# Optimization experiments

Hardware: AMD Instinct MI355X
Metric: run time of the kernel (lower is better)

Reference implementation:

```python
import jax, jax.numpy as jnp
import numpy as np

B, S, D = 128, 50, 128
NUM_NODE = 40000
SAMPLE = 12
HOP = 2
ALPHA = 0.2  # leaky-relu slope (opt.alpha)


def _leaky(x, slope=ALPHA):
    return jnp.where(x >= 0, x, slope * x)


def setup_inputs() -> dict:
    key = jax.random.key(0)
    ks = jax.random.split(key, 12)
    stdv = 1.0 / float(np.sqrt(D))
    inputs = jax.random.randint(ks[0], (B, S), 0, NUM_NODE)
    adj = jax.random.randint(ks[1], (B, S, S), 0, 5)
    mask_item = jax.random.randint(ks[2], (B, S), 0, 2).at[:, 0].set(1)
    item = jax.random.randint(ks[3], (B, S), 0, NUM_NODE)
    adj_all = jax.random.randint(ks[4], (NUM_NODE, SAMPLE), 0, NUM_NODE)
    num_weight = jax.random.uniform(ks[5], (NUM_NODE, SAMPLE), dtype=jnp.float32)
    embedding = jax.random.uniform(ks[6], (NUM_NODE, D), minval=-stdv, maxval=stdv, dtype=jnp.float32)
    a_local = jax.random.uniform(ks[7], (4, D), minval=-stdv, maxval=stdv, dtype=jnp.float32)
    agg_w1 = jax.random.uniform(ks[8], (HOP, D + 1, D), minval=-stdv, maxval=stdv, dtype=jnp.float32)
    agg_w2 = jax.random.uniform(ks[9], (HOP, D, 1), minval=-stdv, maxval=stdv, dtype=jnp.float32)
    agg_w3 = jax.random.uniform(ks[10], (HOP, 2 * D, D), minval=-stdv, maxval=stdv, dtype=jnp.float32)
    return dict(inputs=inputs, adj=adj, mask_item=mask_item, item=item,
                adj_all=adj_all, num_weight=num_weight, embedding=embedding,
                a_local=a_local, agg_w1=agg_w1, agg_w2=agg_w2, agg_w3=agg_w3)


def _local_agg(h, adj, a_local):
    # e_k[b,i,j] = leakyrelu(sum_d h[b,i,d]*h[b,j,d]*a_k[d]); never materialize [B,N,N,D]
    e = _leaky(jnp.einsum('bid,bjd,kd->kbij', h, h, a_local))  # [4,B,S,S]
    alpha = jnp.full(e.shape[1:], -9e15, dtype=h.dtype)
    for k in range(4):
        alpha = jnp.where(adj == k + 1, e[k], alpha)
    alpha = jax.nn.softmax(alpha, axis=-1)
    return alpha @ h


def _global_agg(w1, w2, w3, self_v, neigh_v, neigh_w, extra):
    # self_v [B,L,D]; neigh_v [B,L,SAMPLE,D]; neigh_w [B,L,SAMPLE]; extra [B,L,D]
    feat = jnp.concatenate([extra[:, :, None, :] * neigh_v, neigh_w[..., None]], axis=-1)  # [B,L,SAMPLE,D+1]
    a = _leaky(feat @ w1, 0.2)                              # [B,L,SAMPLE,D]
    a = jax.nn.softmax((a @ w2)[..., 0], axis=-1)[..., None]  # [B,L,SAMPLE,1]
    neigh = jnp.sum(a * neigh_v, axis=-2)                   # [B,L,D]
    out = jnp.concatenate([self_v, neigh], axis=-1) @ w3    # [B,L,D]
    return jax.nn.relu(out)


def _forward(inputs, adj, mask_item, item, adj_all, num_weight, embedding,
             a_local, agg_w1, agg_w2, agg_w3):
    h = embedding[inputs]                          # [B,S,D]
    h_local = _local_agg(h, adj, a_local)
    # multi-hop neighbor sampling (index_select into adj_all / num)
    item_neighbors = [inputs]
    weight_neighbors = []
    support = S
    for _ in range(HOP):
        last = item_neighbors[-1].reshape(-1)
        support *= SAMPLE
        item_neighbors.append(adj_all[last].reshape(B, support))
        weight_neighbors.append(num_weight[last].reshape(B, support))
    entity = [embedding[idx] for idx in item_neighbors]
    mask_f = mask_item.astype(h.dtype)
    item_emb = embedding[item] * mask_f[..., None]
    session = (jnp.sum(item_emb, 1) / jnp.sum(mask_f, -1, keepdims=True))[:, None, :]  # [B,1,D]
    for n_hop in range(HOP):
        nxt = []
        for hop in range(HOP - n_hop):
            self_v = entity[hop]
            L = self_v.shape[1]
            neigh_v = entity[hop + 1].reshape(B, L, SAMPLE, D)
            neigh_w = weight_neighbors[hop].reshape(B, L, SAMPLE)
            extra = jnp.broadcast_to(session, (B, L, D))
            nxt.append(_global_agg(agg_w1[n_hop], agg_w2[n_hop], agg_w3[n_hop],
                                   self_v, neigh_v, neigh_w, extra))
        entity = nxt
    h_global = entity[0].reshape(B, S, D)
    # dropout_local / dropout_global are identity in eval mode
    return h_local + h_global


def reference(inputs, adj, mask_item, item, adj_all, num_weight, embedding,
              a_local, agg_w1, agg_w2, agg_w3):
    return _forward(inputs, adj, mask_item, item, adj_all, num_weight, embedding,
                    a_local, agg_w1, agg_w2, agg_w3)
```

## Files before the change

### kernel.cpp

```cpp
#include <hip/hip_runtime.h>
#include <math.h>

#define BATCH 128
#define S 50
#define D 128
#define SAMPLE 12
#define NL 8

typedef __attribute__((ext_vector_type(8))) short short8v;
typedef __attribute__((ext_vector_type(4))) float f32x4;

__device__ __forceinline__ float leakyf(float x) { return x >= 0.f ? x : 0.2f * x; }
__device__ __forceinline__ unsigned short f2bf(float f) {
    union { float f; unsigned int u; } v; v.f = f;
    unsigned int u = v.u;
    return (unsigned short)((u + 0x7FFFu + ((u >> 16) & 1u)) >> 16);
}
__device__ __forceinline__ float bf2f(unsigned short h) {
    union { float f; unsigned int u; } v; v.u = ((unsigned int)h) << 16; return v.f;
}

__global__ __launch_bounds__(256) void local_agg_kernel(
    const int* __restrict__ inputs, const int* __restrict__ adj,
    const float* __restrict__ emb, const float* __restrict__ a_local,
    float* __restrict__ out)
{
    __shared__ float h[S][D];
    __shared__ float al[4][D];
    __shared__ float alpha[S][S];
    const int b = blockIdx.x;
    const int t = threadIdx.x;

    for (int idx = t; idx < S * D; idx += 256) {
        int i = idx / D, d = idx % D;
        h[i][d] = emb[inputs[b * S + i] * D + d];
    }
    for (int idx = t; idx < 4 * D; idx += 256) al[idx / D][idx % D] = a_local[idx];
    __syncthreads();

    for (int p = t; p < S * S; p += 256) {
        int i = p / S, j = p % S;
        int a = adj[b * S * S + p];
        float v = -9e15f;
        if (a >= 1 && a <= 4) {
            const float* ak = al[a - 1];
            float dot = 0.f;
            #pragma unroll 4
            for (int d = 0; d < D; ++d) dot += h[i][d] * h[j][d] * ak[d];
            v = leakyf(dot);
        }
        alpha[i][j] = v;
    }
    __syncthreads();

    if (t < S) {
        float m = -INFINITY;
        for (int j = 0; j < S; ++j) m = fmaxf(m, alpha[t][j]);
        float ssum = 0.f;
        for (int j = 0; j < S; ++j) { float e = expf(alpha[t][j] - m); alpha[t][j] = e; ssum += e; }
        float inv = 1.f / ssum;
        for (int j = 0; j < S; ++j) alpha[t][j] *= inv;
    }
    __syncthreads();

    for (int idx = t; idx < S * D; idx += 256) {
        int i = idx / D, d = idx % D;
        float acc = 0.f;
        #pragma unroll 5
        for (int j = 0; j < S; ++j) acc += alpha[i][j] * h[j][d];
        out[b * S * D + idx] = acc;
    }
}

__global__ __launch_bounds__(128) void session_kernel(
    const int* __restrict__ item, const int* __restrict__ mask,
    const float* __restrict__ emb, float* __restrict__ session)
{
    const int b = blockIdx.x, d = threadIdx.x;
    float num = 0.f, den = 0.f;
    for (int s = 0; s < S; ++s) {
        float m = (float)mask[b * S + s];
        num += m * emb[item[b * S + s] * D + d];
        den += m;
    }
    session[b * D + d] = num / den;
}

__global__ __launch_bounds__(256) void n1_kernel(
    const int* __restrict__ inputs, const int* __restrict__ adj_all,
    int* __restrict__ n1)
{
    int idx = blockIdx.x * 256 + threadIdx.x;
    if (idx >= BATCH * 600) return;
    int b = idx / 600, j = idx % 600;
    int node = inputs[b * S + j / SAMPLE];
    n1[idx] = adj_all[node * SAMPLE + j % SAMPLE];
}

__global__ __launch_bounds__(256) void prep_kernel(
    const float* __restrict__ w1, const float* __restrict__ w3,
    unsigned short* __restrict__ w1t, unsigned short* __restrict__ w3t)
{
    int idx = blockIdx.x * 256 + threadIdx.x;
    if (idx < 2 * 128 * 128) {
        int h = idx >> 14, r = idx & 16383, n = r >> 7, k = r & 127;
        w1t[idx] = f2bf(w1[h * 129 * 128 + k * 128 + n]);
    } else {
        int j = idx - 2 * 128 * 128;
        int h = j >> 15, r = j & 32767, n = r >> 8, k = r & 255;
        w3t[j] = f2bf(w3[h * 256 * 128 + k * 128 + n]);
    }
}

template <int MODE>
__global__ __launch_bounds__(256, 2) void global_kernel(
    const int* __restrict__ inputs, const int* __restrict__ adj_all,
    const float* __restrict__ num_weight, const float* __restrict__ emb,
    const int* __restrict__ n1, const float* __restrict__ session,
    const unsigned short* __restrict__ ent_self, const unsigned short* __restrict__ ent_neigh,
    const unsigned short* __restrict__ w1t, const float* __restrict__ w1,
    const float* __restrict__ w2, const unsigned short* __restrict__ w3t,
    unsigned short* __restrict__ outb, float* __restrict__ outf, int L)
{
    __shared__ unsigned short nvL[96 * 128];
    __shared__ unsigned short A2[16 * 256];
    __shared__ float score_w[4][96];
    __shared__ float score[96];
    __shared__ float sessL[128];
    __shared__ float w1lastL[128];
    __shared__ float nwgtL[96];
    __shared__ int   selfNode[8];
    __shared__ int   neighIdx[96];

    const int b = blockIdx.y;
    const int l0 = blockIdx.x * NL;
    const int t = threadIdx.x;
    const int lane = t & 63;
    const int wv = t >> 6;
    const int cn = lane & 15;
    const int cg = lane >> 4;

    if (t < 128) sessL[t] = session[b * 128 + t];
    else         w1lastL[t - 128] = w1[128 * 128 + (t - 128)];
    if (t < 8) {
        int l = l0 + t;
        selfNode[t] = (l < L) ? ((MODE == 1) ? n1[b * 600 + l] : inputs[b * S + l]) : -1;
    }
    __syncthreads();

    if (t < 96) {
        int li = t / SAMPLE, s2 = t % SAMPLE;
        int node = selfNode[li];
        int row = -1; float wgt = 0.f;
        if (node >= 0) {
            if (MODE == 0)      row = n1[b * 600 + (l0 + li) * SAMPLE + s2];
            else if (MODE == 1) row = adj_all[node * SAMPLE + s2];
            else                row = b * 600 + (l0 + li) * SAMPLE + s2;
            wgt = num_weight[node * SAMPLE + s2];
        }
        neighIdx[t] = row; nwgtL[t] = wgt;
    }
    reinterpret_cast<float4*>((char*)A2 + 8 * 512)[t] = make_float4(0.f, 0.f, 0.f, 0.f);
    __syncthreads();

    for (int q = t; q < 96 * 32; q += 256) {
        int m = q >> 5, dq = q & 31;
        int row = neighIdx[m];
        ushort4 bv = make_ushort4(0, 0, 0, 0);
        if (row >= 0) {
            if (MODE == 2) {
                bv = reinterpret_cast<const ushort4*>(ent_neigh)[row * 32 + dq];
            } else {
                float4 v = reinterpret_cast<const float4*>(emb)[row * 32 + dq];
                bv.x = f2bf(v.x); bv.y = f2bf(v.y); bv.z = f2bf(v.z); bv.w = f2bf(v.w);
            }
        }
        unsigned byteoff = m * 256 + ((dq * 8) ^ ((m & 7) << 4));
        *reinterpret_cast<ushort4*>((char*)nvL + byteoff) = bv;
    }
    {
        int li = t >> 5, dq = t & 31;
        int l = l0 + li;
        ushort4 bv = make_ushort4(0, 0, 0, 0);
        if (l < L) {
            if (MODE == 2) {
                bv = reinterpret_cast<const ushort4*>(ent_self)[(b * 50 + l) * 32 + dq];
            } else {
                float4 v = reinterpret_cast<const float4*>(emb)[selfNode[li] * 32 + dq];
                bv.x = f2bf(v.x); bv.y = f2bf(v.y); bv.z = f2bf(v.z); bv.w = f2bf(v.w);
            }
        }
        unsigned byteoff = li * 512 + ((dq * 8) ^ ((li & 7) << 4));
        *reinterpret_cast<ushort4*>((char*)A2 + byteoff) = bv;
    }
    __syncthreads();

    f32x4 acc[6][2];
    #pragma unroll
    for (int mt = 0; mt < 6; ++mt)
        #pragma unroll
        for (int j = 0; j < 2; ++j)
            acc[mt][j] = (f32x4){0.f, 0.f, 0.f, 0.f};

    #pragma unroll
    for (int kk = 0; kk < 4; ++kk) {
        int kbase = kk * 32 + cg * 8;
        short8v bfr[2];
        #pragma unroll
        for (int j = 0; j < 2; ++j) {
            int n = (2 * wv + j) * 16 + cn;
            short8v braw = *reinterpret_cast<const short8v*>(w1t + n * 128 + kbase);
            short8v bs;
            #pragma unroll
            for (int e = 0; e < 8; ++e) {
                float f = bf2f((unsigned short)braw[e]) * sessL[kbase + e];
                bs[e] = (short)f2bf(f);
            }
            bfr[j] = bs;
        }
        #pragma unroll
        for (int mt = 0; mt < 6; ++mt) {
            unsigned byteoff = (mt * 16 + cn) * 256 + ((kbase * 2) ^ ((cn & 7) << 4));
            short8v a = *reinterpret_cast<const short8v*>((const char*)nvL + byteoff);
            acc[mt][0] = __builtin_amdgcn_mfma_f32_16x16x32_bf16(a, bfr[0], acc[mt][0], 0, 0, 0);
            acc[mt][1] = __builtin_amdgcn_mfma_f32_16x16x32_bf16(a, bfr[1], acc[mt][1], 0, 0, 0);
        }
    }

    {
        float w2v0 = w2[(2 * wv) * 16 + cn];
        float w2v1 = w2[(2 * wv + 1) * 16 + cn];
        float w1l0 = w1lastL[(2 * wv) * 16 + cn];
        float w1l1 = w1lastL[(2 * wv + 1) * 16 + cn];
        #pragma unroll
        for (int mt = 0; mt < 6; ++mt) {
            #pragma unroll
            for (int r = 0; r < 4; ++r) {
                float nw = nwgtL[mt * 16 + cg * 4 + r];
                float z0 = acc[mt][0][r] + nw * w1l0;
                float z1 = acc[mt][1][r] + nw * w1l1;
                float v = leakyf(z0) * w2v0 + leakyf(z1) * w2v1;
                v += __shfl_xor(v, 1); v += __shfl_xor(v, 2);
                v += __shfl_xor(v, 4); v += __shfl_xor(v, 8);
                if (cn == 0) score_w[wv][mt * 16 + cg * 4 + r] = v;
            }
        }
    }
    __syncthreads();

    if (t < 8) {
        float e[SAMPLE]; float mx = -INFINITY;
        #pragma unroll
        for (int s2 = 0; s2 < SAMPLE; ++s2) {
            int m = t * SAMPLE + s2;
            float v = score_w[0][m] + score_w[1][m] + score_w[2][m] + score_w[3][m];
            e[s2] = v; mx = fmaxf(mx, v);
        }
        float ssum = 0.f;
        #pragma unroll
        for (int s2 = 0; s2 < SAMPLE; ++s2) { e[s2] = expf(e[s2] - mx); ssum += e[s2]; }
        float inv = 1.f / ssum;
        #pragma unroll
        for (int s2 = 0; s2 < SAMPLE; ++s2) score[t * SAMPLE + s2] = e[s2] * inv;
    }
    __syncthreads();

    #pragma unroll
    for (int i = 0; i < 4; ++i) {
        int idx = i * 256 + t;
        int l = idx >> 7, d = idx & 127;
        float a = 0.f;
        #pragma unroll
        for (int s2 = 0; s2 < SAMPLE; ++s2) {
            int m = l * SAMPLE + s2;
            unsigned byteoff = m * 256 + ((2 * d) ^ ((m & 7) << 4));
            a += score[m] * bf2f(*reinterpret_cast<const unsigned short*>((const char*)nvL + byteoff));
        }
        unsigned ob = l * 512 + ((2 * (128 + d)) ^ ((l & 7) << 4));
        *reinterpret_cast<unsigned short*>((char*)A2 + ob) = f2bf(a);
    }
    __syncthreads();

    f32x4 acc2[2];
    acc2[0] = (f32x4){0.f, 0.f, 0.f, 0.f};
    acc2[1] = (f32x4){0.f, 0.f, 0.f, 0.f};
    #pragma unroll
    for (int kk = 0; kk < 8; ++kk) {
        int kbase = kk * 32 + cg * 8;
        unsigned ab = cn * 512 + ((kbase * 2) ^ ((cn & 7) << 4));
        short8v a = *reinterpret_cast<const short8v*>((const char*)A2 + ab);
        #pragma unroll
        for (int j = 0; j < 2; ++j) {
            int n = (2 * wv + j) * 16 + cn;
            short8v bb = *reinterpret_cast<const short8v*>(w3t + n * 256 + kbase);
            acc2[j] = __builtin_amdgcn_mfma_f32_16x16x32_bf16(a, bb, acc2[j], 0, 0, 0);
        }
    }
    #pragma unroll
    for (int j = 0; j < 2; ++j) {
        int n = (2 * wv + j) * 16 + cn;
        #pragma unroll
        for (int r = 0; r < 4; ++r) {
            int rowi = cg * 4 + r;
            if (rowi < 8 && (l0 + rowi) < L) {
                float val = fmaxf(acc2[j][r], 0.f);
                if (MODE == 2) {
                    float* p = outf + ((size_t)(b * 50) + l0 + rowi) * 128 + n;
                    *p = val + *p;
                } else {
                    outb[((size_t)b * L + l0 + rowi) * 128 + n] = f2bf(val);
                }
            }
        }
    }
}

extern "C" void kernel_launch(void* const* d_in, const int* in_sizes, int n_in,
                              void* d_out, int out_size, void* d_ws, size_t ws_size,
                              hipStream_t stream)
{
    const int*   inputs     = (const int*)d_in[0];
    const int*   adj        = (const int*)d_in[1];
    const int*   mask_item  = (const int*)d_in[2];
    const int*   item       = (const int*)d_in[3];
    const int*   adj_all    = (const int*)d_in[4];
    const float* num_weight = (const float*)d_in[5];
    const float* embedding  = (const float*)d_in[6];
    const float* a_local    = (const float*)d_in[7];
    const float* agg_w1     = (const float*)d_in[8];
    const float* agg_w2     = (const float*)d_in[9];
    const float* agg_w3     = (const float*)d_in[10];
    float* out = (float*)d_out;

    float*          ws_session = (float*)d_ws;
    int*            ws_n1      = (int*)(ws_session + 16384);
    unsigned short* ws_w1t     = (unsigned short*)(ws_n1 + 76800);
    unsigned short* ws_w3t     = ws_w1t + 2 * 128 * 128;
    unsigned short* ws_out0    = ws_w3t + 2 * 128 * 256;
    unsigned short* ws_out1    = ws_out0 + (size_t)BATCH * 50 * D;

    prep_kernel<<<dim3(384), 256, 0, stream>>>(agg_w1, agg_w3, ws_w1t, ws_w3t);
    local_agg_kernel<<<dim3(BATCH), 256, 0, stream>>>(inputs, adj, embedding, a_local, out);
    session_kernel<<<dim3(BATCH), 128, 0, stream>>>(item, mask_item, embedding, ws_session);
    n1_kernel<<<dim3(300), 256, 0, stream>>>(inputs, adj_all, ws_n1);

    global_kernel<0><<<dim3(7, BATCH), 256, 0, stream>>>(
        inputs, adj_all, num_weight, embedding, ws_n1, ws_session,
        nullptr, nullptr, ws_w1t, agg_w1, agg_w2, ws_w3t, ws_out0, nullptr, 50);
    global_kernel<1><<<dim3(75, BATCH), 256, 0, stream>>>(
        inputs, adj_all, num_weight, embedding, ws_n1, ws_session,
        nullptr, nullptr, ws_w1t, agg_w1, agg_w2, ws_w3t, ws_out1, nullptr, 600);
    global_kernel<2><<<dim3(7, BATCH), 256, 0, stream>>>(
        inputs, adj_all, num_weight, embedding, ws_n1, ws_session,
        ws_out0, ws_out1, ws_w1t + 128 * 128, agg_w1 + 129 * 128,
        agg_w2 + 128, ws_w3t + 128 * 256, nullptr, out, 50);
}
```

Measured before the change: 355.5 us.

## Fuse local and hop-0 global kernels, pre-convert embedding and session-scaled W1 to bf16

Replaces the seven launches with four. Session and n1 are merged into one setup kernel. A prep kernel converts the whole embedding table to bf16 and builds per-batch session-scaled W1 tiles. The local aggregation and both hop-0 global paths share one launch, picked by block index. Gathers become 16-byte bf16 loads, the B fragments no longer need per-element rescaling, the weighted-sum loop handles two values per thread, and occupancy is raised to 4 blocks per CU. In exchange, the whole 40000x128 table is converted every call, which costs about 30MB of traffic.

```diff
diff --git a/kernel.cpp b/kernel.cpp
--- a/kernel.cpp
+++ b/kernel.cpp
@@ -5,146 +5,171 @@
 #define S 50
 #define D 128
 #define SAMPLE 12
-#define NL 8
 
 typedef __attribute__((ext_vector_type(8))) short short8v;
 typedef __attribute__((ext_vector_type(4))) float f32x4;
+typedef unsigned short u16;
 
 __device__ __forceinline__ float leakyf(float x) { return x >= 0.f ? x : 0.2f * x; }
-__device__ __forceinline__ unsigned short f2bf(float f) {
-    union { float f; unsigned int u; } v; v.f = f;
-    unsigned int u = v.u;
-    return (unsigned short)((u + 0x7FFFu + ((u >> 16) & 1u)) >> 16);
-}
-__device__ __forceinline__ float bf2f(unsigned short h) {
-    union { float f; unsigned int u; } v; v.u = ((unsigned int)h) << 16; return v.f;
-}
-
-__global__ __launch_bounds__(256) void local_agg_kernel(
+__device__ __forceinline__ u16 f2bf(float f) {
+    union { float f; unsigned u; } v; v.f = f;
+    unsigned u = v.u;
+    return (u16)((u + 0x7FFFu + ((u >> 16) & 1u)) >> 16);
+}
+__device__ __forceinline__ float bf2f(u16 h) {
+    union { float f; unsigned u; } v; v.u = ((unsigned)h) << 16; return v.f;
+}
+
+__global__ __launch_bounds__(256) void setup_kernel(
+    const int* __restrict__ item, const int* __restrict__ mask,
+    const int* __restrict__ inputs, const int* __restrict__ adj_all,
+    const float* __restrict__ emb, float* __restrict__ session, int* __restrict__ n1)
+{
+    const int bx = blockIdx.x, t = threadIdx.x;
+    if (bx < BATCH) {
+        if (t < 128) {
+            float num = 0.f, den = 0.f;
+            for (int s = 0; s < S; ++s) {
+                float m = (float)mask[bx * S + s];
+                num += m * emb[item[bx * S + s] * D + t];
+                den += m;
+            }
+            session[bx * D + t] = num / den;
+        }
+    } else {
+        int idx = (bx - BATCH) * 256 + t;
+        if (idx < BATCH * 600) {
+            int b = idx / 600, j = idx % 600;
+            n1[idx] = adj_all[inputs[b * S + j / SAMPLE] * SAMPLE + j % SAMPLE];
+        }
+    }
+}
+
+__global__ __launch_bounds__(256) void prep_kernel(
+    const float* __restrict__ emb, const float* __restrict__ w1,
+    const float* __restrict__ w3, const float* __restrict__ session,
+    u16* __restrict__ emb_bf, u16* __restrict__ sw1, u16* __restrict__ w3t)
+{
+    const int bx = blockIdx.x, t = threadIdx.x;
+    if (bx < 2500) {
+        int idx = bx * 256 + t;
+        const float4* src = reinterpret_cast<const float4*>(emb) + (size_t)idx * 2;
+        float4 a = src[0], c = src[1];
+        u16 o[8] = {f2bf(a.x), f2bf(a.y), f2bf(a.z), f2bf(a.w),
+                    f2bf(c.x), f2bf(c.y), f2bf(c.z), f2bf(c.w)};
+        *reinterpret_cast<uint4*>(emb_bf + (size_t)idx * 8) = *reinterpret_cast<uint4*>(o);
+    } else if (bx < 2756) {
+        int id = bx - 2500, hop = id >> 7, b = id & 127;
+        const float* w1s = w1 + hop * 129 * 128;
+        const float* se = session + b * 128;
+        int n = t >> 1, kh = (t & 1) * 64;
+        u16* dst = sw1 + (((size_t)(hop * 128 + b) * 128 + n) * 128) + kh;
+        for (int kq = 0; kq < 64; kq += 8) {
+            u16 o[8];
+            #pragma unroll
+            for (int e = 0; e < 8; ++e) { int k = kh + kq + e; o[e] = f2bf(w1s[k * 128 + n] * se[k]); }
+            *reinterpret_cast<uint4*>(dst + kq) = *reinterpret_cast<uint4*>(o);
+        }
+    } else {
+        int j = (bx - 2756) * 256 + t;
+        int hop = j >> 12, r = j & 4095, n = r >> 5, k0 = (r & 31) * 8;
+        const float* w3s = w3 + hop * 256 * 128;
+        u16 o[8];
+        #pragma unroll
+        for (int e = 0; e < 8; ++e) o[e] = f2bf(w3s[(k0 + e) * 128 + n]);
+        *reinterpret_cast<uint4*>(w3t + ((size_t)hop * 128 + n) * 256 + k0) = *reinterpret_cast<uint4*>(o);
+    }
+}
+
+template <int PATH>
+__global__ __launch_bounds__(256, 4) void main_kernel(
     const int* __restrict__ inputs, const int* __restrict__ adj,
+    const int* __restrict__ adj_all, const float* __restrict__ num_weight,
     const float* __restrict__ emb, const float* __restrict__ a_local,
-    float* __restrict__ out)
+    const int* __restrict__ n1,
+    const u16* __restrict__ emb_bf, const u16* __restrict__ sw1,
+    const float* __restrict__ w1, const float* __restrict__ w2,
+    const u16* __restrict__ w3t,
+    const u16* __restrict__ in0, const u16* __restrict__ in1,
+    u16* __restrict__ o0, u16* __restrict__ o1, float* __restrict__ outf)
 {
-    __shared__ float h[S][D];
-    __shared__ float al[4][D];
-    __shared__ float alpha[S][S];
-    const int b = blockIdx.x;
+    __shared__ __align__(16) char smem[37664];
+    const int b = blockIdx.y;
     const int t = threadIdx.x;
-
-    for (int idx = t; idx < S * D; idx += 256) {
-        int i = idx / D, d = idx % D;
-        h[i][d] = emb[inputs[b * S + i] * D + d];
-    }
-    for (int idx = t; idx < 4 * D; idx += 256) al[idx / D][idx % D] = a_local[idx];
-    __syncthreads();
-
-    for (int p = t; p < S * S; p += 256) {
-        int i = p / S, j = p % S;
-        int a = adj[b * S * S + p];
-        float v = -9e15f;
-        if (a >= 1 && a <= 4) {
-            const float* ak = al[a - 1];
-            float dot = 0.f;
-            #pragma unroll 4
-            for (int d = 0; d < D; ++d) dot += h[i][d] * h[j][d] * ak[d];
-            v = leakyf(dot);
-        }
-        alpha[i][j] = v;
-    }
-    __syncthreads();
-
-    if (t < S) {
-        float m = -INFINITY;
-        for (int j = 0; j < S; ++j) m = fmaxf(m, alpha[t][j]);
-        float ssum = 0.f;
-        for (int j = 0; j < S; ++j) { float e = expf(alpha[t][j] - m); alpha[t][j] = e; ssum += e; }
-        float inv = 1.f / ssum;
-        for (int j = 0; j < S; ++j) alpha[t][j] *= inv;
-    }
-    __syncthreads();
-
-    for (int idx = t; idx < S * D; idx += 256) {
-        int i = idx / D, d = idx % D;
-        float acc = 0.f;
-        #pragma unroll 5
-        for (int j = 0; j < S; ++j) acc += alpha[i][j] * h[j][d];
-        out[b * S * D + idx] = acc;
-    }
-}
-
-__global__ __launch_bounds__(128) void session_kernel(
-    const int* __restrict__ item, const int* __restrict__ mask,
-    const float* __restrict__ emb, float* __restrict__ session)
-{
-    const int b = blockIdx.x, d = threadIdx.x;
-    float num = 0.f, den = 0.f;
-    for (int s = 0; s < S; ++s) {
-        float m = (float)mask[b * S + s];
-        num += m * emb[item[b * S + s] * D + d];
-        den += m;
-    }
-    session[b * D + d] = num / den;
-}
-
-__global__ __launch_bounds__(256) void n1_kernel(
-    const int* __restrict__ inputs, const int* __restrict__ adj_all,
-    int* __restrict__ n1)
-{
-    int idx = blockIdx.x * 256 + threadIdx.x;
-    if (idx >= BATCH * 600) return;
-    int b = idx / 600, j = idx % 600;
-    int node = inputs[b * S + j / SAMPLE];
-    n1[idx] = adj_all[node * SAMPLE + j % SAMPLE];
-}
-
-__global__ __launch_bounds__(256) void prep_kernel(
-    const float* __restrict__ w1, const float* __restrict__ w3,
-    unsigned short* __restrict__ w1t, unsigned short* __restrict__ w3t)
-{
-    int idx = blockIdx.x * 256 + threadIdx.x;
-    if (idx < 2 * 128 * 128) {
-        int h = idx >> 14, r = idx & 16383, n = r >> 7, k = r & 127;
-        w1t[idx] = f2bf(w1[h * 129 * 128 + k * 128 + n]);
-    } else {
-        int j = idx - 2 * 128 * 128;
-        int h = j >> 15, r = j & 32767, n = r >> 8, k = r & 255;
-        w3t[j] = f2bf(w3[h * 256 * 128 + k * 128 + n]);
-    }
-}
-
-template <int MODE>
-__global__ __launch_bounds__(256, 2) void global_kernel(
-    const int* __restrict__ inputs, const int* __restrict__ adj_all,
-    const float* __restrict__ num_weight, const float* __restrict__ emb,
-    const int* __restrict__ n1, const float* __restrict__ session,
-    const unsigned short* __restrict__ ent_self, const unsigned short* __restrict__ ent_neigh,
-    const unsigned short* __restrict__ w1t, const float* __restrict__ w1,
-    const float* __restrict__ w2, const unsigned short* __restrict__ w3t,
-    unsigned short* __restrict__ outb, float* __restrict__ outf, int L)
-{
-    __shared__ unsigned short nvL[96 * 128];
-    __shared__ unsigned short A2[16 * 256];
-    __shared__ float score_w[4][96];
-    __shared__ float score[96];
-    __shared__ float sessL[128];
-    __shared__ float w1lastL[128];
-    __shared__ float nwgtL[96];
-    __shared__ int   selfNode[8];
-    __shared__ int   neighIdx[96];
-
-    const int b = blockIdx.y;
-    const int l0 = blockIdx.x * NL;
-    const int t = threadIdx.x;
-    const int lane = t & 63;
-    const int wv = t >> 6;
-    const int cn = lane & 15;
-    const int cg = lane >> 4;
-
-    if (t < 128) sessL[t] = session[b * 128 + t];
-    else         w1lastL[t - 128] = w1[128 * 128 + (t - 128)];
+    const int bx = blockIdx.x;
+
+    if (PATH == 0 && bx == 82) {
+        float (*h)[D]     = (float(*)[D])smem;
+        float (*al)[D]    = (float(*)[D])(smem + 25600);
+        float (*alpha)[S] = (float(*)[S])(smem + 27648);
+
+        for (int idx = t; idx < S * D; idx += 256) {
+            int i = idx / D, d = idx % D;
+            h[i][d] = emb[inputs[b * S + i] * D + d];
+        }
+        for (int idx = t; idx < 4 * D; idx += 256) al[idx / D][idx % D] = a_local[idx];
+        __syncthreads();
+
+        for (int p = t; p < S * S; p += 256) {
+            int i = p / S, j = p % S;
+            int a = adj[b * S * S + p];
+            float v = -9e15f;
+            if (a >= 1 && a <= 4) {
+                const float* ak = al[a - 1];
+                float dot = 0.f;
+                #pragma unroll 4
+                for (int d = 0; d < D; ++d) dot += h[i][d] * h[j][d] * ak[d];
+                v = leakyf(dot);
+            }
+            alpha[i][j] = v;
+        }
+        __syncthreads();
+
+        if (t < S) {
+            float m = -INFINITY;
+            for (int j = 0; j < S; ++j) m = fmaxf(m, alpha[t][j]);
+            float ssum = 0.f;
+            for (int j = 0; j < S; ++j) { float e = expf(alpha[t][j] - m); alpha[t][j] = e; ssum += e; }
+            float inv = 1.f / ssum;
+            for (int j = 0; j < S; ++j) alpha[t][j] *= inv;
+        }
+        __syncthreads();
+
+        for (int idx = t; idx < S * D; idx += 256) {
+            int i = idx / D, d = idx % D;
+            float acc = 0.f;
+            #pragma unroll 5
+            for (int j = 0; j < S; ++j) acc += alpha[i][j] * h[j][d];
+            outf[b * S * D + idx] = acc;
+        }
+        return;
+    }
+
+    int mode, l0, L, hop;
+    const u16 *nsrc, *ssrc;
+    u16* outb;
+    if (PATH == 2)      { mode = 2; l0 = bx * 8;        L = 50;  nsrc = in1;    ssrc = in0;    outb = nullptr; hop = 1; }
+    else if (bx < 75)   { mode = 1; l0 = bx * 8;        L = 600; nsrc = emb_bf; ssrc = emb_bf; outb = o1;      hop = 0; }
+    else                { mode = 0; l0 = (bx - 75) * 8; L = 50;  nsrc = emb_bf; ssrc = emb_bf; outb = o0;      hop = 0; }
+
+    u16* nvL = (u16*)smem;
+    u16* A2  = (u16*)(smem + 24576);
+    float (*score_w)[96] = (float(*)[96])(smem + 32768);
+    float* score    = (float*)(smem + 34304);
+    float* nwgt     = (float*)(smem + 34688);
+    int*   neighIdx = (int*)(smem + 35072);
+    int*   selfNode = (int*)(smem + 35456);
+
+    const u16*   sw1b   = sw1 + (size_t)(hop * 128 + b) * 16384;
+    const float* w1last = w1 + hop * 129 * 128 + 128 * 128;
+    const float* w2h    = w2 + hop * 128;
+    const u16*   w3th   = w3t + hop * 32768;
+
+    const int lane = t & 63, wv = t >> 6, cn = lane & 15, cg = lane >> 4;
+
     if (t < 8) {
         int l = l0 + t;
-        selfNode[t] = (l < L) ? ((MODE == 1) ? n1[b * 600 + l] : inputs[b * S + l]) : -1;
+        selfNode[t] = (l < L) ? ((mode == 1) ? n1[b * 600 + l] : inputs[b * S + l]) : -1;
     }
     __syncthreads();
 
@@ -153,93 +178,69 @@
         int node = selfNode[li];
         int row = -1; float wgt = 0.f;
         if (node >= 0) {
-            if (MODE == 0)      row = n1[b * 600 + (l0 + li) * SAMPLE + s2];
-            else if (MODE == 1) row = adj_all[node * SAMPLE + s2];
+            if (mode == 0)      row = n1[b * 600 + (l0 + li) * SAMPLE + s2];
+            else if (mode == 1) row = adj_all[node * SAMPLE + s2];
             else                row = b * 600 + (l0 + li) * SAMPLE + s2;
             wgt = num_weight[node * SAMPLE + s2];
         }
-        neighIdx[t] = row; nwgtL[t] = wgt;
-    }
-    reinterpret_cast<float4*>((char*)A2 + 8 * 512)[t] = make_float4(0.f, 0.f, 0.f, 0.f);
-    __syncthreads();
-
-    for (int q = t; q < 96 * 32; q += 256) {
-        int m = q >> 5, dq = q & 31;
+        neighIdx[t] = row; nwgt[t] = wgt;
+    }
+    *reinterpret_cast<uint4*>((char*)A2 + 8 * 512 + t * 16) = make_uint4(0, 0, 0, 0);
+    __syncthreads();
+
+    #pragma unroll
+    for (int i = 0; i < 6; ++i) {
+        int q = i * 256 + t;
+        int m = q >> 4, dq = q & 15;
         int row = neighIdx[m];
-        ushort4 bv = make_ushort4(0, 0, 0, 0);
-        if (row >= 0) {
-            if (MODE == 2) {
-                bv = reinterpret_cast<const ushort4*>(ent_neigh)[row * 32 + dq];
-            } else {
-                float4 v = reinterpret_cast<const float4*>(emb)[row * 32 + dq];
-                bv.x = f2bf(v.x); bv.y = f2bf(v.y); bv.z = f2bf(v.z); bv.w = f2bf(v.w);
-            }
-        }
-        unsigned byteoff = m * 256 + ((dq * 8) ^ ((m & 7) << 4));
-        *reinterpret_cast<ushort4*>((char*)nvL + byteoff) = bv;
-    }
-    {
-        int li = t >> 5, dq = t & 31;
+        uint4 v = make_uint4(0, 0, 0, 0);
+        if (row >= 0) v = *reinterpret_cast<const uint4*>(nsrc + (size_t)row * 128 + dq * 8);
+        *reinterpret_cast<uint4*>((char*)nvL + m * 256 + ((dq * 16) ^ ((m & 7) << 4))) = v;
+    }
+    if (t < 128) {
+        int li = t >> 4, dq = t & 15;
         int l = l0 + li;
-        ushort4 bv = make_ushort4(0, 0, 0, 0);
+        uint4 v = make_uint4(0, 0, 0, 0);
         if (l < L) {
-            if (MODE == 2) {
-                bv = reinterpret_cast<const ushort4*>(ent_self)[(b * 50 + l) * 32 + dq];
-            } else {
-                float4 v = reinterpret_cast<const float4*>(emb)[selfNode[li] * 32 + dq];
-                bv.x = f2bf(v.x); bv.y = f2bf(v.y); bv.z = f2bf(v.z); bv.w = f2bf(v.w);
-            }
-        }
-        unsigned byteoff = li * 512 + ((dq * 8) ^ ((li & 7) << 4));
-        *reinterpret_cast<ushort4*>((char*)A2 + byteoff) = bv;
+            int srow = (mode == 2) ? (b * 50 + l) : selfNode[li];
+            v = *reinterpret_cast<const uint4*>(ssrc + (size_t)srow * 128 + dq * 8);
+        }
+        *reinterpret_cast<uint4*>((char*)A2 + li * 512 + ((dq * 16) ^ ((li & 7) << 4))) = v;
     }
     __syncthreads();
 
     f32x4 acc[6][2];
     #pragma unroll
-    for (int mt = 0; mt < 6; ++mt)
-        #pragma unroll
-        for (int j = 0; j < 2; ++j)
-            acc[mt][j] = (f32x4){0.f, 0.f, 0.f, 0.f};
-
+    for (int mt = 0; mt < 6; ++mt) {
+        acc[mt][0] = (f32x4){0.f, 0.f, 0.f, 0.f};
+        acc[mt][1] = (f32x4){0.f, 0.f, 0.f, 0.f};
+    }
     #pragma unroll
     for (int kk = 0; kk < 4; ++kk) {
         int kbase = kk * 32 + cg * 8;
-        short8v bfr[2];
-        #pragma unroll
-        for (int j = 0; j < 2; ++j) {
-            int n = (2 * wv + j) * 16 + cn;
-            short8v braw = *reinterpret_cast<const short8v*>(w1t + n * 128 + kbase);
-            short8v bs;
-            #pragma unroll
-            for (int e = 0; e < 8; ++e) {
-                float f = bf2f((unsigned short)braw[e]) * sessL[kbase + e];
-                bs[e] = (short)f2bf(f);
-            }
-            bfr[j] = bs;
-        }
+        short8v b0 = *reinterpret_cast<const short8v*>(sw1b + ((2 * wv) * 16 + cn) * 128 + kbase);
+        short8v b1 = *reinterpret_cast<const short8v*>(sw1b + ((2 * wv + 1) * 16 + cn) * 128 + kbase);
         #pragma unroll
         for (int mt = 0; mt < 6; ++mt) {
-            unsigned byteoff = (mt * 16 + cn) * 256 + ((kbase * 2) ^ ((cn & 7) << 4));
-            short8v a = *reinterpret_cast<const short8v*>((const char*)nvL + byteoff);
-            acc[mt][0] = __builtin_amdgcn_mfma_f32_16x16x32_bf16(a, bfr[0], acc[mt][0], 0, 0, 0);
-            acc[mt][1] = __builtin_amdgcn_mfma_f32_16x16x32_bf16(a, bfr[1], acc[mt][1], 0, 0, 0);
+            short8v a = *reinterpret_cast<const short8v*>(
+                (const char*)nvL + (mt * 16 + cn) * 256 + ((kbase * 2) ^ ((cn & 7) << 4)));
+            acc[mt][0] = __builtin_amdgcn_mfma_f32_16x16x32_bf16(a, b0, acc[mt][0], 0, 0, 0);
+            acc[mt][1] = __builtin_amdgcn_mfma_f32_16x16x32_bf16(a, b1, acc[mt][1], 0, 0, 0);
         }
     }
 
     {
-        float w2v0 = w2[(2 * wv) * 16 + cn];
-        float w2v1 = w2[(2 * wv + 1) * 16 + cn];
-        float w1l0 = w1lastL[(2 * wv) * 16 + cn];
-        float w1l1 = w1lastL[(2 * wv + 1) * 16 + cn];
+        float w2v0 = w2h[(2 * wv) * 16 + cn];
+        float w2v1 = w2h[(2 * wv + 1) * 16 + cn];
+        float w1l0 = w1last[(2 * wv) * 16 + cn];
+        float w1l1 = w1last[(2 * wv + 1) * 16 + cn];
         #pragma unroll
         for (int mt = 0; mt < 6; ++mt) {
             #pragma unroll
             for (int r = 0; r < 4; ++r) {
-                float nw = nwgtL[mt * 16 + cg * 4 + r];
-                float z0 = acc[mt][0][r] + nw * w1l0;
-                float z1 = acc[mt][1][r] + nw * w1l1;
-                float v = leakyf(z0) * w2v0 + leakyf(z1) * w2v1;
+                float nw = nwgt[mt * 16 + cg * 4 + r];
+                float v = leakyf(acc[mt][0][r] + nw * w1l0) * w2v0 +
+                          leakyf(acc[mt][1][r] + nw * w1l1) * w2v1;
                 v += __shfl_xor(v, 1); v += __shfl_xor(v, 2);
                 v += __shfl_xor(v, 4); v += __shfl_xor(v, 8);
                 if (cn == 0) score_w[wv][mt * 16 + cg * 4 + r] = v;
@@ -266,18 +267,21 @@
     __syncthreads();
 
     #pragma unroll
-    for (int i = 0; i < 4; ++i) {
+    for (int i = 0; i < 2; ++i) {
         int idx = i * 256 + t;
-        int l = idx >> 7, d = idx & 127;
-        float a = 0.f;
+        int l = idx >> 6, d2 = idx & 63;
+        float a0 = 0.f, a1 = 0.f;
         #pragma unroll
         for (int s2 = 0; s2 < SAMPLE; ++s2) {
             int m = l * SAMPLE + s2;
-            unsigned byteoff = m * 256 + ((2 * d) ^ ((m & 7) << 4));
-            a += score[m] * bf2f(*reinterpret_cast<const unsigned short*>((const char*)nvL + byteoff));
-        }
-        unsigned ob = l * 512 + ((2 * (128 + d)) ^ ((l & 7) << 4));
-        *reinterpret_cast<unsigned short*>((char*)A2 + ob) = f2bf(a);
+            unsigned pk = *reinterpret_cast<const unsigned*>(
+                (const char*)nvL + m * 256 + ((4 * d2) ^ ((m & 7) << 4)));
+            float sc = score[m];
+            a0 += sc * bf2f((u16)(pk & 0xffff));
+            a1 += sc * bf2f((u16)(pk >> 16));
+        }
+        unsigned packed = ((unsigned)f2bf(a1) << 16) | f2bf(a0);
+        *reinterpret_cast<unsigned*>((char*)A2 + l * 512 + ((256 + 4 * d2) ^ ((l & 7) << 4))) = packed;
     }
     __syncthreads();
 
@@ -287,14 +291,12 @@
     #pragma unroll
     for (int kk = 0; kk < 8; ++kk) {
         int kbase = kk * 32 + cg * 8;
-        unsigned ab = cn * 512 + ((kbase * 2) ^ ((cn & 7) << 4));
-        short8v a = *reinterpret_cast<const short8v*>((const char*)A2 + ab);
-        #pragma unroll
-        for (int j = 0; j < 2; ++j) {
-            int n = (2 * wv + j) * 16 + cn;
-            short8v bb = *reinterpret_cast<const short8v*>(w3t + n * 256 + kbase);
-            acc2[j] = __builtin_amdgcn_mfma_f32_16x16x32_bf16(a, bb, acc2[j], 0, 0, 0);
-        }
+        short8v a = *reinterpret_cast<const short8v*>(
+            (const char*)A2 + cn * 512 + ((kbase * 2) ^ ((cn & 7) << 4)));
+        short8v bb0 = *reinterpret_cast<const short8v*>(w3th + ((2 * wv) * 16 + cn) * 256 + kbase);
+        short8v bb1 = *reinterpret_cast<const short8v*>(w3th + ((2 * wv + 1) * 16 + cn) * 256 + kbase);
+        acc2[0] = __builtin_amdgcn_mfma_f32_16x16x32_bf16(a, bb0, acc2[0], 0, 0, 0);
+        acc2[1] = __builtin_amdgcn_mfma_f32_16x16x32_bf16(a, bb1, acc2[1], 0, 0, 0);
     }
     #pragma unroll
     for (int j = 0; j < 2; ++j) {
@@ -304,7 +306,7 @@
             int rowi = cg * 4 + r;
             if (rowi < 8 && (l0 + rowi) < L) {
                 float val = fmaxf(acc2[j][r], 0.f);
-                if (MODE == 2) {
+                if (PATH == 2) {
                     float* p = outf + ((size_t)(b * 50) + l0 + rowi) * 128 + n;
                     *p = val + *p;
                 } else {
@@ -332,26 +334,27 @@
     const float* agg_w3     = (const float*)d_in[10];
     float* out = (float*)d_out;
 
-    float*          ws_session = (float*)d_ws;
-    int*            ws_n1      = (int*)(ws_session + 16384);
-    unsigned short* ws_w1t     = (unsigned short*)(ws_n1 + 76800);
-    unsigned short* ws_w3t     = ws_w1t + 2 * 128 * 128;
-    unsigned short* ws_out0    = ws_w3t + 2 * 128 * 256;
-    unsigned short* ws_out1    = ws_out0 + (size_t)BATCH * 50 * D;
-
-    prep_kernel<<<dim3(384), 256, 0, stream>>>(agg_w1, agg_w3, ws_w1t, ws_w3t);
-    local_agg_kernel<<<dim3(BATCH), 256, 0, stream>>>(inputs, adj, embedding, a_local, out);
-    session_kernel<<<dim3(BATCH), 128, 0, stream>>>(item, mask_item, embedding, ws_session);
-    n1_kernel<<<dim3(300), 256, 0, stream>>>(inputs, adj_all, ws_n1);
-
-    global_kernel<0><<<dim3(7, BATCH), 256, 0, stream>>>(
-        inputs, adj_all, num_weight, embedding, ws_n1, ws_session,
-        nullptr, nullptr, ws_w1t, agg_w1, agg_w2, ws_w3t, ws_out0, nullptr, 50);
-    global_kernel<1><<<dim3(75, BATCH), 256, 0, stream>>>(
-        inputs, adj_all, num_weight, embedding, ws_n1, ws_session,
-        nullptr, nullptr, ws_w1t, agg_w1, agg_w2, ws_w3t, ws_out1, nullptr, 600);
-    global_kernel<2><<<dim3(7, BATCH), 256, 0, stream>>>(
-        inputs, adj_all, num_weight, embedding, ws_n1, ws_session,
-        ws_out0, ws_out1, ws_w1t + 128 * 128, agg_w1 + 129 * 128,
-        agg_w2 + 128, ws_w3t + 128 * 256, nullptr, out, 50);
-}
+    char* w = (char*)d_ws;
+    float* ws_session = (float*)(w);
+    int*   ws_n1      = (int*)(w + 65536);
+    u16*   ws_emb     = (u16*)(w + 372736);
+    u16*   ws_sw1     = (u16*)(w + 10612736);
+    u16*   ws_w3t     = (u16*)(w + 19001344);
+    u16*   ws_out0    = (u16*)(w + 19132416);
+    u16*   ws_out1    = (u16*)(w + 20770816);
+
+    setup_kernel<<<dim3(BATCH + 300), 256, 0, stream>>>(
+        item, mask_item, inputs, adj_all, embedding, ws_session, ws_n1);
+    prep_kernel<<<dim3(2788), 256, 0, stream>>>(
+        embedding, agg_w1, agg_w3, ws_session, ws_emb, ws_sw1, ws_w3t);
+
+    main_kernel<0><<<dim3(83, BATCH), 256, 0, stream>>>(
+        inputs, adj, adj_all, num_weight, embedding, a_local, ws_n1,
+        ws_emb, ws_sw1, agg_w1, agg_w2, ws_w3t,
+        nullptr, nullptr, ws_out0, ws_out1, out);
+
+    main_kernel<2><<<dim3(7, BATCH), 256, 0, stream>>>(
+        inputs, adj, adj_all, num_weight, embedding, a_local, ws_n1,
+        ws_emb, ws_sw1, agg_w1, agg_w2, ws_w3t,
+        ws_out0, ws_out1, nullptr, nullptr, out);
+}
```

Result: faster. 330.4 us (-7.1%).
